# Optimization experiments

Measured on AMD Instinct MI355X. Metric: run time of the kernel, lower is better.

## Reference

```python
import jax, jax.numpy as jnp
import numpy as np

N = 50000   # vertices
E = 25000   # hyperedges
NNZ = 400000  # incidence pairs (v, e)
D_IN = 512
D_OUT = 512  # heads * out_channels, heads=1


def setup_inputs() -> dict:
    key = jax.random.key(0)
    kx, kw, kv, ke = jax.random.split(key, 4)
    X = jax.random.normal(kx, (N, D_IN), dtype=jnp.float32)
    W = jax.random.normal(kw, (D_OUT, D_IN), dtype=jnp.float32) * 0.02  # nn.Linear weight [out,in]
    vidx = jax.random.randint(kv, (NNZ,), 0, N, dtype=jnp.int32)
    eidx = jax.random.randint(ke, (NNZ,), 0, E, dtype=jnp.int32)
    # degE = 1/|e| (hyperedge size), degV = 1/deg(v), as precomputed by hyperg
    ones = jnp.ones((NNZ,), dtype=jnp.float32)
    edge_sz = jax.ops.segment_sum(ones, eidx, num_segments=E)
    vert_dg = jax.ops.segment_sum(ones, vidx, num_segments=N)
    degE = 1.0 / jnp.maximum(edge_sz, 1.0)
    degV = 1.0 / jnp.maximum(vert_dg, 1.0)
    Wdiag = jnp.ones((E,), dtype=jnp.float32)
    return {"X": X, "W": W, "degE": degE, "degV": degV, "Wdiag": Wdiag,
            "vidx": vidx, "eidx": eidx}


def reference(X, W, degE, degV, Wdiag, vidx, eidx):
    # Dense projection: X @ W^T (nn.Linear, no bias)
    Xp = jnp.einsum('nd,od->no', X, W)                      # [N, D_OUT]
    # Stage 1: vertex -> hyperedge (first_aggr: mean via degE), weighted by Wdiag
    Xe = jax.ops.segment_sum(Xp[vidx], eidx, num_segments=E)  # [E, D_OUT]
    Xe = Xe * (degE * Wdiag)[:, None]
    # Stage 2: hyperedge -> vertex, normalized by degV
    Xv = jax.ops.segment_sum(Xe[eidx], vidx, num_segments=N)  # [N, D_OUT]
    Xv = Xv * degV[:, None]
    return Xv
```

## Files before the change

kernel.cpp:

```cpp
#include <hip/hip_runtime.h>

typedef unsigned short u16;
typedef unsigned int   u32;
typedef __attribute__((ext_vector_type(4))) float f32x4;
typedef __attribute__((ext_vector_type(4))) u32   u32x4;
typedef __attribute__((ext_vector_type(8))) __bf16 bf16x8;

constexpr int NV   = 50000;
constexpr int NE   = 25000;
constexpr int NNZp = 400000;
constexpr int D    = 512;
constexpr int MP2  = 25088;
constexpr int NBE  = 25;
constexpr int NBV  = 49;
constexpr int SG1  = 391;
constexpr int SG2  = 1563;

static __device__ __forceinline__ u16 f2bf(float f) {
  u32 u = __float_as_uint(f);
  u32 r = (u + 0x7fffu + ((u >> 16) & 1u)) >> 16;
  return (u16)r;
}
static __device__ __forceinline__ u32 pk2(float a, float b) {
  return (u32)f2bf(a) | ((u32)f2bf(b) << 16);
}

static __device__ __forceinline__ void gload_lds16(const u16* g, u16* l) {
  __builtin_amdgcn_global_load_lds(
      (const __attribute__((address_space(1))) u32*)g,
      (__attribute__((address_space(3))) u32*)l, 16, 0, 0);
}

__global__ void zero_kernel(int* cntE, int* cntV) {
  int i = blockIdx.x * 256 + threadIdx.x;
  if (i < NE) cntE[i] = 0;
  if (i < NV) cntV[i] = 0;
}

__global__ void hist_kernel(const int* __restrict__ vidx, const int* __restrict__ eidx,
                            int* cntE, int* cntV) {
  int i = blockIdx.x * 256 + threadIdx.x;
  if (i < NNZp) {
    atomicAdd(&cntE[eidx[i]], 1);
    atomicAdd(&cntV[vidx[i]], 1);
  }
}

__global__ __launch_bounds__(256) void scan1_kernel(
    const int* __restrict__ cntE, const int* __restrict__ cntV,
    int* offE, int* offV, int* blkSum) {
  const bool isE = blockIdx.x < NBE;
  const int* cnt = isE ? cntE : cntV;
  int* off = isE ? offE : offV;
  const int len = isE ? NE : NV;
  const int t = threadIdx.x;
  const int base = (isE ? blockIdx.x : blockIdx.x - NBE) * 1024 + t * 4;
  int4 c = {0, 0, 0, 0};
  if (base + 4 <= len) c = *(const int4*)(cnt + base);
  else {
    if (base + 0 < len) c.x = cnt[base + 0];
    if (base + 1 < len) c.y = cnt[base + 1];
    if (base + 2 < len) c.z = cnt[base + 2];
    if (base + 3 < len) c.w = cnt[base + 3];
  }
  int s = c.x + c.y + c.z + c.w;
  __shared__ int sm[256];
  sm[t] = s;
  __syncthreads();
  for (int d = 1; d < 256; d <<= 1) {
    int u = (t >= d) ? sm[t - d] : 0;
    __syncthreads();
    sm[t] += u;
    __syncthreads();
  }
  int ex = sm[t] - s;
  int4 o;
  o.x = ex; o.y = o.x + c.x; o.z = o.y + c.y; o.w = o.z + c.z;
  if (base + 4 <= len) *(int4*)(off + base) = o;
  else {
    if (base + 0 < len) off[base + 0] = o.x;
    if (base + 1 < len) off[base + 1] = o.y;
    if (base + 2 < len) off[base + 2] = o.z;
    if (base + 3 < len) off[base + 3] = o.w;
  }
  if (t == 255) blkSum[blockIdx.x] = sm[255];
}

__global__ void scan2_kernel(int* blkSum) {
  int wv = threadIdx.x >> 6, lane = threadIdx.x & 63;
  int off = wv ? NBE : 0, len = wv ? NBV : NBE;
  int v = (lane < len) ? blkSum[off + lane] : 0;
  int incl = v;
#pragma unroll
  for (int d = 1; d < 64; d <<= 1) {
    int u = __shfl_up(incl, d, 64);
    if (lane >= d) incl += u;
  }
  if (lane < len) blkSum[off + lane] = incl - v;
}

__global__ __launch_bounds__(256) void scan3_kernel(
    int* offE, int* offV, int* curE, int* curV, const int* __restrict__ blkSum) {
  const bool isE = blockIdx.x < NBE;
  int* off = isE ? offE : offV;
  int* cur = isE ? curE : curV;
  const int len = isE ? NE : NV;
  const int pref = blkSum[blockIdx.x];
  const int base = (isE ? blockIdx.x : blockIdx.x - NBE) * 1024 + threadIdx.x * 4;
  if (base + 4 <= len) {
    int4 o = *(int4*)(off + base);
    o.x += pref; o.y += pref; o.z += pref; o.w += pref;
    *(int4*)(off + base) = o;
    *(int4*)(cur + base) = o;
  } else {
    for (int q = 0; q < 4; q++)
      if (base + q < len) { int v = off[base + q] + pref; off[base + q] = v; cur[base + q] = v; }
  }
}

__global__ void scatter_kernel(const int* __restrict__ vidx, const int* __restrict__ eidx,
                               int* curE, int* curV, int* csr_ev, int* csr_ve) {
  int i = blockIdx.x * 256 + threadIdx.x;
  if (i < NNZp) {
    int e = eidx[i], v = vidx[i];
    csr_ev[atomicAdd(&curE[e], 1)] = v;
    csr_ve[atomicAdd(&curV[v], 1)] = e;
  }
}

__global__ __launch_bounds__(256) void convert_kernel(
    const float* __restrict__ X, const float* __restrict__ W,
    u16* __restrict__ Xb, u16* __restrict__ Wb) {
  constexpr size_t NX = (size_t)NV * D;
  size_t i = ((size_t)blockIdx.x * 256 + threadIdx.x) * 8;
  const float* src;
  u16* dst;
  if (i < NX) {
    int n = (int)(i >> 9);
    int col = (int)(i & 511);
    int t = col >> 5, w = col & 31;
    src = X + i;
    dst = Xb + (size_t)t * NV * 32 + (size_t)n * 32 + w;
  } else {
    src = W + (i - NX);
    dst = Wb + (i - NX);
  }
  f32x4 a = *(const f32x4*)src;
  f32x4 b = *(const f32x4*)(src + 4);
  u32x4 p = { pk2(a[0], a[1]), pk2(a[2], a[3]), pk2(b[0], b[1]), pk2(b[2], b[3]) };
  *(u32x4*)dst = p;
}

__global__ __launch_bounds__(256) void stage1_kernel(
    const u16* __restrict__ Xb, const int* __restrict__ offE, const int* __restrict__ cntE,
    const int* __restrict__ csr_ev, u16* __restrict__ XeR) {
  const int wave = threadIdx.x >> 6;
  const int lane = threadIdx.x & 63;
  const int g    = lane >> 2;
  const int c    = lane & 3;
  const int bid  = blockIdx.x;
  const int xcd  = bid & 7;
  const int tmp  = bid >> 3;
  const int phase = (tmp >= SG1) ? 1 : 0;
  const int sg    = tmp - phase * SG1;
  const int t     = xcd + 8 * phase;
  const int e     = sg * 64 + wave * 16 + g;
  const u16* base = Xb + (size_t)t * NV * 32;
  int start = 0, cnt = 0;
  if (e < NE) { start = offE[e]; cnt = cntE[e]; }
  float acc[8] = {};
  for (int j0 = 0; j0 < cnt; j0 += 4) {
    int idx = (j0 + c < cnt) ? csr_ev[start + j0 + c] : 0;
    int kmax = min(4, cnt - j0);
    for (int k = 0; k < kmax; k++) {
      int v = __shfl(idx, (lane & ~3) | k, 64);
      u32x4 p = *(const u32x4*)(base + (size_t)v * 32 + c * 8);
#pragma unroll
      for (int q = 0; q < 4; q++) {
        u32 u = p[q];
        acc[2 * q]     += __uint_as_float(u << 16);
        acc[2 * q + 1] += __uint_as_float(u & 0xffff0000u);
      }
    }
  }
  if (e < NE) {
    u32x4 o = { pk2(acc[0], acc[1]), pk2(acc[2], acc[3]),
                pk2(acc[4], acc[5]), pk2(acc[6], acc[7]) };
    *(u32x4*)(XeR + (size_t)e * D + t * 32 + c * 8) = o;
  }
}

__global__ __launch_bounds__(256) void gemm_kernel(const u16* __restrict__ A,
                                                   const u16* __restrict__ B,
                                                   const float* __restrict__ degE,
                                                   const float* __restrict__ Wdiag,
                                                   u16* __restrict__ C) {
  __shared__ u16 sA[128 * 32];
  __shared__ u16 sB[128 * 32];
  const int tid  = threadIdx.x;
  const int lane = tid & 63;
  const int wave = tid >> 6;
  const int bm = blockIdx.y * 128;
  const int bn = blockIdx.x * 128;
  const int wm = (wave >> 1) * 64;
  const int wn = (wave & 1) * 64;
  const int lr = lane & 15;
  const int lk = (lane >> 4) * 8;
  const int srow = lane >> 2;
  const int scol = (lane & 3) * 8;

  f32x4 acc[4][4] = {};

  for (int kt = 0; kt < D; kt += 32) {
    __syncthreads();
#pragma unroll
    for (int c = 0; c < 2; c++) {
      const int ar = wave * 16 + c * 64;
      gload_lds16(A + (size_t)(bm + ar + srow) * D + kt + scol, &sA[ar * 32]);
      gload_lds16(B + (size_t)(bn + ar + srow) * D + kt + scol, &sB[ar * 32]);
    }
    __syncthreads();

    bf16x8 af[4], bfr[4];
#pragma unroll
    for (int i = 0; i < 4; i++) af[i]  = *(const bf16x8*)&sA[(wm + i * 16 + lr) * 32 + lk];
#pragma unroll
    for (int j = 0; j < 4; j++) bfr[j] = *(const bf16x8*)&sB[(wn + j * 16 + lr) * 32 + lk];
#pragma unroll
    for (int i = 0; i < 4; i++)
#pragma unroll
      for (int j = 0; j < 4; j++)
        acc[i][j] = __builtin_amdgcn_mfma_f32_16x16x32_bf16(af[i], bfr[j], acc[i][j], 0, 0, 0);
  }

#pragma unroll
  for (int i = 0; i < 4; i++)
#pragma unroll
    for (int r = 0; r < 4; r++) {
      int row = bm + wm + i * 16 + (lane >> 4) * 4 + r;
      if (row < NE) {
        float se = degE[row] * Wdiag[row];
#pragma unroll
        for (int j = 0; j < 4; j++) {
          int col = bn + wn + lr + j * 16;
          int s = col >> 6, w = col & 63;
          C[(size_t)s * MP2 * 64 + (size_t)row * 64 + w] = f2bf(acc[i][j][r] * se);
        }
      }
    }
}

__global__ __launch_bounds__(256) void stage2_kernel(
    const u16* __restrict__ Xe2, const int* __restrict__ offV, const int* __restrict__ cntV,
    const int* __restrict__ csr_ve, const float* __restrict__ degV, float* __restrict__ out) {
  const int wave = threadIdx.x >> 6;
  const int lane = threadIdx.x & 63;
  const int g    = lane >> 3;
  const int c    = lane & 7;
  const int s    = blockIdx.x & 7;
  const int sg   = blockIdx.x >> 3;
  const int v    = sg * 32 + wave * 8 + g;
  const u16* base = Xe2 + (size_t)s * MP2 * 64;
  int start = 0, cnt = 0;
  if (v < NV) { start = offV[v]; cnt = cntV[v]; }
  float acc[8] = {};
  for (int j0 = 0; j0 < cnt; j0 += 8) {
    int idx = (j0 + c < cnt) ? csr_ve[start + j0 + c] : 0;
    int kmax = min(8, cnt - j0);
    for (int k = 0; k < kmax; k++) {
      int e = __shfl(idx, (lane & ~7) | k, 64);
      u32x4 p = *(const u32x4*)(base + (size_t)e * 64 + c * 8);
#pragma unroll
      for (int q = 0; q < 4; q++) {
        u32 u = p[q];
        acc[2 * q]     += __uint_as_float(u << 16);
        acc[2 * q + 1] += __uint_as_float(u & 0xffff0000u);
      }
    }
  }
  if (v < NV) {
    float sc = degV[v];
    float* orow = out + (size_t)v * D + s * 64 + c * 8;
    f32x4 o0 = { acc[0] * sc, acc[1] * sc, acc[2] * sc, acc[3] * sc };
    f32x4 o1 = { acc[4] * sc, acc[5] * sc, acc[6] * sc, acc[7] * sc };
    *(f32x4*)orow = o0;
    *(f32x4*)(orow + 4) = o1;
  }
}

extern "C" void kernel_launch(void* const* d_in, const int* in_sizes, int n_in,
                              void* d_out, int out_size, void* d_ws, size_t ws_size,
                              hipStream_t stream) {
  const float* X     = (const float*)d_in[0];
  const float* W     = (const float*)d_in[1];
  const float* degE  = (const float*)d_in[2];
  const float* degV  = (const float*)d_in[3];
  const float* Wdiag = (const float*)d_in[4];
  const int*   vidx  = (const int*)d_in[5];
  const int*   eidx  = (const int*)d_in[6];
  float* out = (float*)d_out;

  char* p = (char*)d_ws;
  auto take = [&](size_t bytes) { char* r = p; p += (bytes + 255) & ~(size_t)255; return r; };
  u16* Xb     = (u16*)take((size_t)NV * D * 2);
  u16* Wb     = (u16*)take((size_t)D * D * 2);
  u16* XeR    = (u16*)take((size_t)MP2 * D * 2);
  u16* Xe2    = (u16*)take((size_t)MP2 * D * 2);
  int* cntE   = (int*)take((size_t)NE * 4);
  int* offE   = (int*)take((size_t)NE * 4);
  int* curE   = (int*)take((size_t)NE * 4);
  int* cntV   = (int*)take((size_t)NV * 4);
  int* offV   = (int*)take((size_t)NV * 4);
  int* curV   = (int*)take((size_t)NV * 4);
  int* csr_ev = (int*)take((size_t)NNZp * 4);
  int* csr_ve = (int*)take((size_t)NNZp * 4);
  int* blkSum = (int*)take((size_t)(NBE + NBV) * 4);

  constexpr size_t NCONV = ((size_t)NV * D + (size_t)D * D) / 8 / 256;

  zero_kernel   <<<(NV + 255) / 256, 256, 0, stream>>>(cntE, cntV);
  hist_kernel   <<<(NNZp + 255) / 256, 256, 0, stream>>>(vidx, eidx, cntE, cntV);
  scan1_kernel  <<<NBE + NBV, 256, 0, stream>>>(cntE, cntV, offE, offV, blkSum);
  scan2_kernel  <<<1, 128, 0, stream>>>(blkSum);
  scan3_kernel  <<<NBE + NBV, 256, 0, stream>>>(offE, offV, curE, curV, blkSum);
  scatter_kernel<<<(NNZp + 255) / 256, 256, 0, stream>>>(vidx, eidx, curE, curV, csr_ev, csr_ve);
  convert_kernel<<<NCONV, 256, 0, stream>>>(X, W, Xb, Wb);
  stage1_kernel <<<SG1 * 16, 256, 0, stream>>>(Xb, offE, cntE, csr_ev, XeR);
  gemm_kernel   <<<dim3(D / 128, MP2 / 128), 256, 0, stream>>>(XeR, Wb, degE, Wdiag, Xe2);
  stage2_kernel <<<SG2 * 8, 256, 0, stream>>>(Xe2, offV, cntV, csr_ve, degV, out);
}
```

Baseline: 434.2 us.

## Use row-major layouts and one-wave-per-row gathers with batched loads

Drops the column-slab tiled layouts of Xb and Xe2 in favour of plain row-major storage. Each wave now handles one hyperedge or vertex, and its 64 lanes cover the full 512-wide row, so every gathered row is one contiguous 1 KB read. Eight gathered rows are loaded into registers before accumulating, to keep more memory requests in flight. The cost is that the slab layout, which kept each XCD's working set to one column slice for L2 locality, is gone, and per-row load imbalance now falls on whole waves.

```diff
diff --git a/kernel.cpp b/kernel.cpp
--- a/kernel.cpp
+++ b/kernel.cpp
@@ -13,8 +13,6 @@
 constexpr int MP2  = 25088;
 constexpr int NBE  = 25;
 constexpr int NBV  = 49;
-constexpr int SG1  = 391;
-constexpr int SG2  = 1563;
 
 static __device__ __forceinline__ u16 f2bf(float f) {
   u32 u = __float_as_uint(f);
@@ -136,11 +134,8 @@
   const float* src;
   u16* dst;
   if (i < NX) {
-    int n = (int)(i >> 9);
-    int col = (int)(i & 511);
-    int t = col >> 5, w = col & 31;
     src = X + i;
-    dst = Xb + (size_t)t * NV * 32 + (size_t)n * 32 + w;
+    dst = Xb + i;
   } else {
     src = W + (i - NX);
     dst = Wb + (i - NX);
@@ -156,38 +151,59 @@
     const int* __restrict__ csr_ev, u16* __restrict__ XeR) {
   const int wave = threadIdx.x >> 6;
   const int lane = threadIdx.x & 63;
-  const int g    = lane >> 2;
-  const int c    = lane & 3;
-  const int bid  = blockIdx.x;
-  const int xcd  = bid & 7;
-  const int tmp  = bid >> 3;
-  const int phase = (tmp >= SG1) ? 1 : 0;
-  const int sg    = tmp - phase * SG1;
-  const int t     = xcd + 8 * phase;
-  const int e     = sg * 64 + wave * 16 + g;
-  const u16* base = Xb + (size_t)t * NV * 32;
-  int start = 0, cnt = 0;
-  if (e < NE) { start = offE[e]; cnt = cntE[e]; }
+  const int e = blockIdx.x * 4 + wave;
+  if (e >= NE) return;
+  const int start = offE[e];
+  const int cnt   = cntE[e];
   float acc[8] = {};
-  for (int j0 = 0; j0 < cnt; j0 += 4) {
-    int idx = (j0 + c < cnt) ? csr_ev[start + j0 + c] : 0;
-    int kmax = min(4, cnt - j0);
-    for (int k = 0; k < kmax; k++) {
-      int v = __shfl(idx, (lane & ~3) | k, 64);
-      u32x4 p = *(const u32x4*)(base + (size_t)v * 32 + c * 8);
-#pragma unroll
-      for (int q = 0; q < 4; q++) {
-        u32 u = p[q];
-        acc[2 * q]     += __uint_as_float(u << 16);
-        acc[2 * q + 1] += __uint_as_float(u & 0xffff0000u);
-      }
-    }
-  }
-  if (e < NE) {
-    u32x4 o = { pk2(acc[0], acc[1]), pk2(acc[2], acc[3]),
-                pk2(acc[4], acc[5]), pk2(acc[6], acc[7]) };
-    *(u32x4*)(XeR + (size_t)e * D + t * 32 + c * 8) = o;
-  }
+  for (int b = 0; b < cnt; b += 64) {
+    const int n = min(64, cnt - b);
+    int idx = 0;
+    if (lane < n) idx = csr_ev[start + b + lane];
+    int k0 = 0;
+    for (; k0 + 8 <= n; k0 += 8) {
+      u32x4 buf[8];
+#pragma unroll
+      for (int p = 0; p < 8; p++) {
+        int v = __shfl(idx, k0 + p, 64);
+        buf[p] = *(const u32x4*)(Xb + (size_t)v * D + lane * 8);
+      }
+#pragma unroll
+      for (int p = 0; p < 8; p++) {
+#pragma unroll
+        for (int q = 0; q < 4; q++) {
+          u32 u = buf[p][q];
+          acc[2 * q]     += __uint_as_float(u << 16);
+          acc[2 * q + 1] += __uint_as_float(u & 0xffff0000u);
+        }
+      }
+    }
+    const int rem = n - k0;
+    if (rem) {
+      u32x4 buf[8];
+#pragma unroll
+      for (int p = 0; p < 8; p++) {
+        if (p < rem) {
+          int v = __shfl(idx, k0 + p, 64);
+          buf[p] = *(const u32x4*)(Xb + (size_t)v * D + lane * 8);
+        }
+      }
+#pragma unroll
+      for (int p = 0; p < 8; p++) {
+        if (p < rem) {
+#pragma unroll
+          for (int q = 0; q < 4; q++) {
+            u32 u = buf[p][q];
+            acc[2 * q]     += __uint_as_float(u << 16);
+            acc[2 * q + 1] += __uint_as_float(u & 0xffff0000u);
+          }
+        }
+      }
+    }
+  }
+  u32x4 o = { pk2(acc[0], acc[1]), pk2(acc[2], acc[3]),
+              pk2(acc[4], acc[5]), pk2(acc[6], acc[7]) };
+  *(u32x4*)(XeR + (size_t)e * D + lane * 8) = o;
 }
 
 __global__ __launch_bounds__(256) void gemm_kernel(const u16* __restrict__ A,
@@ -243,8 +259,7 @@
 #pragma unroll
         for (int j = 0; j < 4; j++) {
           int col = bn + wn + lr + j * 16;
-          int s = col >> 6, w = col & 63;
-          C[(size_t)s * MP2 * 64 + (size_t)row * 64 + w] = f2bf(acc[i][j][r] * se);
+          C[(size_t)row * D + col] = f2bf(acc[i][j][r] * se);
         }
       }
     }
@@ -255,37 +270,62 @@
     const int* __restrict__ csr_ve, const float* __restrict__ degV, float* __restrict__ out) {
   const int wave = threadIdx.x >> 6;
   const int lane = threadIdx.x & 63;
-  const int g    = lane >> 3;
-  const int c    = lane & 7;
-  const int s    = blockIdx.x & 7;
-  const int sg   = blockIdx.x >> 3;
-  const int v    = sg * 32 + wave * 8 + g;
-  const u16* base = Xe2 + (size_t)s * MP2 * 64;
-  int start = 0, cnt = 0;
-  if (v < NV) { start = offV[v]; cnt = cntV[v]; }
+  const int v = blockIdx.x * 4 + wave;
+  if (v >= NV) return;
+  const int start = offV[v];
+  const int cnt   = cntV[v];
   float acc[8] = {};
-  for (int j0 = 0; j0 < cnt; j0 += 8) {
-    int idx = (j0 + c < cnt) ? csr_ve[start + j0 + c] : 0;
-    int kmax = min(8, cnt - j0);
-    for (int k = 0; k < kmax; k++) {
-      int e = __shfl(idx, (lane & ~7) | k, 64);
-      u32x4 p = *(const u32x4*)(base + (size_t)e * 64 + c * 8);
-#pragma unroll
-      for (int q = 0; q < 4; q++) {
-        u32 u = p[q];
-        acc[2 * q]     += __uint_as_float(u << 16);
-        acc[2 * q + 1] += __uint_as_float(u & 0xffff0000u);
-      }
-    }
-  }
-  if (v < NV) {
-    float sc = degV[v];
-    float* orow = out + (size_t)v * D + s * 64 + c * 8;
-    f32x4 o0 = { acc[0] * sc, acc[1] * sc, acc[2] * sc, acc[3] * sc };
-    f32x4 o1 = { acc[4] * sc, acc[5] * sc, acc[6] * sc, acc[7] * sc };
-    *(f32x4*)orow = o0;
-    *(f32x4*)(orow + 4) = o1;
-  }
+  for (int b = 0; b < cnt; b += 64) {
+    const int n = min(64, cnt - b);
+    int idx = 0;
+    if (lane < n) idx = csr_ve[start + b + lane];
+    int k0 = 0;
+    for (; k0 + 8 <= n; k0 += 8) {
+      u32x4 buf[8];
+#pragma unroll
+      for (int p = 0; p < 8; p++) {
+        int e = __shfl(idx, k0 + p, 64);
+        buf[p] = *(const u32x4*)(Xe2 + (size_t)e * D + lane * 8);
+      }
+#pragma unroll
+      for (int p = 0; p < 8; p++) {
+#pragma unroll
+        for (int q = 0; q < 4; q++) {
+          u32 u = buf[p][q];
+          acc[2 * q]     += __uint_as_float(u << 16);
+          acc[2 * q + 1] += __uint_as_float(u & 0xffff0000u);
+        }
+      }
+    }
+    const int rem = n - k0;
+    if (rem) {
+      u32x4 buf[8];
+#pragma unroll
+      for (int p = 0; p < 8; p++) {
+        if (p < rem) {
+          int e = __shfl(idx, k0 + p, 64);
+          buf[p] = *(const u32x4*)(Xe2 + (size_t)e * D + lane * 8);
+        }
+      }
+#pragma unroll
+      for (int p = 0; p < 8; p++) {
+        if (p < rem) {
+#pragma unroll
+          for (int q = 0; q < 4; q++) {
+            u32 u = buf[p][q];
+            acc[2 * q]     += __uint_as_float(u << 16);
+            acc[2 * q + 1] += __uint_as_float(u & 0xffff0000u);
+          }
+        }
+      }
+    }
+  }
+  const float sc = degV[v];
+  float* orow = out + (size_t)v * D + lane * 8;
+  f32x4 o0 = { acc[0] * sc, acc[1] * sc, acc[2] * sc, acc[3] * sc };
+  f32x4 o1 = { acc[4] * sc, acc[5] * sc, acc[6] * sc, acc[7] * sc };
+  *(f32x4*)orow = o0;
+  *(f32x4*)(orow + 4) = o1;
 }
 
 extern "C" void kernel_launch(void* const* d_in, const int* in_sizes, int n_in,
@@ -325,7 +365,7 @@
   scan3_kernel  <<<NBE + NBV, 256, 0, stream>>>(offE, offV, curE, curV, blkSum);
   scatter_kernel<<<(NNZp + 255) / 256, 256, 0, stream>>>(vidx, eidx, curE, curV, csr_ev, csr_ve);
   convert_kernel<<<NCONV, 256, 0, stream>>>(X, W, Xb, Wb);
-  stage1_kernel <<<SG1 * 16, 256, 0, stream>>>(Xb, offE, cntE, csr_ev, XeR);
+  stage1_kernel <<<NE / 4, 256, 0, stream>>>(Xb, offE, cntE, csr_ev, XeR);
   gemm_kernel   <<<dim3(D / 128, MP2 / 128), 256, 0, stream>>>(XeR, Wb, degE, Wdiag, Xe2);
-  stage2_kernel <<<SG2 * 8, 256, 0, stream>>>(Xe2, offV, cntV, csr_ve, degV, out);
-}
+  stage2_kernel <<<NV / 4, 256, 0, stream>>>(Xe2, offV, cntV, csr_ve, degV, out);
+}
```

Measured after the change: 429.8 us. Within noise of the previous version (-1.0%).

## Assign one wave per segment in gather stages with cross-lane butterfly reduction

Applied to the files above, without the earlier changes.

Stage1 and stage2 now give each wave a single hyperedge or vertex instead of 16 or 8 segments per wave. The wave's lane groups walk different neighbours in parallel, and the partial sums are combined with a shfl_xor butterfly reduction that also transposes the columns so each lane stores one scalar. This is meant to remove serial per-segment loops and load imbalance from varying segment sizes, and to raise memory-level parallelism. In exchange it adds shuffle work, turns the vector stores into scalar stores, launches many more blocks, drops the bounds checks on e and v, and uses nontemporal loads for the CSR index arrays.

```diff
diff --git a/kernel.cpp b/kernel.cpp
--- a/kernel.cpp
+++ b/kernel.cpp
@@ -13,8 +13,7 @@
 constexpr int MP2  = 25088;
 constexpr int NBE  = 25;
 constexpr int NBV  = 49;
-constexpr int SG1  = 391;
-constexpr int SG2  = 1563;
+constexpr int EB1  = 6250;
 
 static __device__ __forceinline__ u16 f2bf(float f) {
   u32 u = __float_as_uint(f);
@@ -156,24 +155,23 @@
     const int* __restrict__ csr_ev, u16* __restrict__ XeR) {
   const int wave = threadIdx.x >> 6;
   const int lane = threadIdx.x & 63;
-  const int g    = lane >> 2;
+  const int slot = lane >> 2;
   const int c    = lane & 3;
   const int bid  = blockIdx.x;
   const int xcd  = bid & 7;
   const int tmp  = bid >> 3;
-  const int phase = (tmp >= SG1) ? 1 : 0;
-  const int sg    = tmp - phase * SG1;
+  const int phase = (tmp >= EB1) ? 1 : 0;
+  const int eg    = tmp - phase * EB1;
   const int t     = xcd + 8 * phase;
-  const int e     = sg * 64 + wave * 16 + g;
+  const int e     = eg * 4 + wave;
+  const int start = __builtin_nontemporal_load(offE + e);
+  const int cnt   = __builtin_nontemporal_load(cntE + e);
   const u16* base = Xb + (size_t)t * NV * 32;
-  int start = 0, cnt = 0;
-  if (e < NE) { start = offE[e]; cnt = cntE[e]; }
   float acc[8] = {};
-  for (int j0 = 0; j0 < cnt; j0 += 4) {
-    int idx = (j0 + c < cnt) ? csr_ev[start + j0 + c] : 0;
-    int kmax = min(4, cnt - j0);
-    for (int k = 0; k < kmax; k++) {
-      int v = __shfl(idx, (lane & ~3) | k, 64);
+  for (int j0 = 0; j0 < cnt; j0 += 16) {
+    int j = j0 + slot;
+    if (j < cnt) {
+      int v = __builtin_nontemporal_load(csr_ev + start + j);
       u32x4 p = *(const u32x4*)(base + (size_t)v * 32 + c * 8);
 #pragma unroll
       for (int q = 0; q < 4; q++) {
@@ -183,10 +181,27 @@
       }
     }
   }
-  if (e < NE) {
-    u32x4 o = { pk2(acc[0], acc[1]), pk2(acc[2], acc[3]),
-                pk2(acc[4], acc[5]), pk2(acc[6], acc[7]) };
-    *(u32x4*)(XeR + (size_t)e * D + t * 32 + c * 8) = o;
+#pragma unroll
+  for (int i = 0; i < 4; i++) {
+    float send = (lane & 4) ? acc[i] : acc[i + 4];
+    float keep = (lane & 4) ? acc[i + 4] : acc[i];
+    acc[i] = keep + __shfl_xor(send, 4, 64);
+  }
+#pragma unroll
+  for (int i = 0; i < 2; i++) {
+    float send = (lane & 8) ? acc[i] : acc[i + 2];
+    float keep = (lane & 8) ? acc[i + 2] : acc[i];
+    acc[i] = keep + __shfl_xor(send, 8, 64);
+  }
+  {
+    float send = (lane & 16) ? acc[0] : acc[1];
+    float keep = (lane & 16) ? acc[1] : acc[0];
+    acc[0] = keep + __shfl_xor(send, 16, 64);
+  }
+  acc[0] += __shfl_xor(acc[0], 32, 64);
+  if (!(lane & 32)) {
+    int col = c * 8 + ((lane >> 2) & 1) * 4 + ((lane >> 3) & 1) * 2 + ((lane >> 4) & 1);
+    XeR[(size_t)e * D + t * 32 + col] = f2bf(acc[0]);
   }
 }
 
@@ -255,20 +270,19 @@
     const int* __restrict__ csr_ve, const float* __restrict__ degV, float* __restrict__ out) {
   const int wave = threadIdx.x >> 6;
   const int lane = threadIdx.x & 63;
-  const int g    = lane >> 3;
+  const int slot = lane >> 3;
   const int c    = lane & 7;
   const int s    = blockIdx.x & 7;
-  const int sg   = blockIdx.x >> 3;
-  const int v    = sg * 32 + wave * 8 + g;
+  const int vg   = blockIdx.x >> 3;
+  const int v    = vg * 4 + wave;
+  const int start = __builtin_nontemporal_load(offV + v);
+  const int cnt   = __builtin_nontemporal_load(cntV + v);
   const u16* base = Xe2 + (size_t)s * MP2 * 64;
-  int start = 0, cnt = 0;
-  if (v < NV) { start = offV[v]; cnt = cntV[v]; }
   float acc[8] = {};
   for (int j0 = 0; j0 < cnt; j0 += 8) {
-    int idx = (j0 + c < cnt) ? csr_ve[start + j0 + c] : 0;
-    int kmax = min(8, cnt - j0);
-    for (int k = 0; k < kmax; k++) {
-      int e = __shfl(idx, (lane & ~7) | k, 64);
+    int j = j0 + slot;
+    if (j < cnt) {
+      int e = __builtin_nontemporal_load(csr_ve + start + j);
       u32x4 p = *(const u32x4*)(base + (size_t)e * 64 + c * 8);
 #pragma unroll
       for (int q = 0; q < 4; q++) {
@@ -278,14 +292,26 @@
       }
     }
   }
-  if (v < NV) {
-    float sc = degV[v];
-    float* orow = out + (size_t)v * D + s * 64 + c * 8;
-    f32x4 o0 = { acc[0] * sc, acc[1] * sc, acc[2] * sc, acc[3] * sc };
-    f32x4 o1 = { acc[4] * sc, acc[5] * sc, acc[6] * sc, acc[7] * sc };
-    *(f32x4*)orow = o0;
-    *(f32x4*)(orow + 4) = o1;
-  }
+#pragma unroll
+  for (int i = 0; i < 4; i++) {
+    float send = (lane & 8) ? acc[i] : acc[i + 4];
+    float keep = (lane & 8) ? acc[i + 4] : acc[i];
+    acc[i] = keep + __shfl_xor(send, 8, 64);
+  }
+#pragma unroll
+  for (int i = 0; i < 2; i++) {
+    float send = (lane & 16) ? acc[i] : acc[i + 2];
+    float keep = (lane & 16) ? acc[i + 2] : acc[i];
+    acc[i] = keep + __shfl_xor(send, 16, 64);
+  }
+  {
+    float send = (lane & 32) ? acc[0] : acc[1];
+    float keep = (lane & 32) ? acc[1] : acc[0];
+    acc[0] = keep + __shfl_xor(send, 32, 64);
+  }
+  const float sc = degV[v];
+  int col = c * 8 + ((lane >> 3) & 1) * 4 + ((lane >> 4) & 1) * 2 + ((lane >> 5) & 1);
+  out[(size_t)v * D + s * 64 + col] = acc[0] * sc;
 }
 
 extern "C" void kernel_launch(void* const* d_in, const int* in_sizes, int n_in,
@@ -325,7 +351,7 @@
   scan3_kernel  <<<NBE + NBV, 256, 0, stream>>>(offE, offV, curE, curV, blkSum);
   scatter_kernel<<<(NNZp + 255) / 256, 256, 0, stream>>>(vidx, eidx, curE, curV, csr_ev, csr_ve);
   convert_kernel<<<NCONV, 256, 0, stream>>>(X, W, Xb, Wb);
-  stage1_kernel <<<SG1 * 16, 256, 0, stream>>>(Xb, offE, cntE, csr_ev, XeR);
+  stage1_kernel <<<EB1 * 16, 256, 0, stream>>>(Xb, offE, cntE, csr_ev, XeR);
   gemm_kernel   <<<dim3(D / 128, MP2 / 128), 256, 0, stream>>>(XeR, Wb, degE, Wdiag, Xe2);
-  stage2_kernel <<<SG2 * 8, 256, 0, stream>>>(Xe2, offV, cntV, csr_ve, degV, out);
-}
+  stage2_kernel <<<(NV / 4) * 8, 256, 0, stream>>>(Xe2, offV, cntV, csr_ve, degV, out);
+}
```

Result: slower. 619.6 us (+42.7%).

## Sort rows by degree for load-balanced gathers and batch neighbor index loads

Applied to the files above, without the earlier changes.

Adds a degree histogram, a scan and a counting-sort pass so hyperedges and vertices are processed in degree-sorted order. Rows with similar neighbor counts then share a wave, which is meant to reduce divergence in the stage1 and stage2 gather loops. The inner loops also change: each lane now loads 4 indices directly and issues 4 independent row loads at a time instead of shuffling one index per step, which exposes more memory-level parallelism. The cost is extra small kernels and indirect id lookups, and output writes become scattered rather than in row order.

```diff
diff --git a/kernel.cpp b/kernel.cpp
--- a/kernel.cpp
+++ b/kernel.cpp
@@ -13,8 +13,8 @@
 constexpr int MP2  = 25088;
 constexpr int NBE  = 25;
 constexpr int NBV  = 49;
-constexpr int SG1  = 391;
-constexpr int SG2  = 1563;
+constexpr int BPS1 = 391;
+constexpr int BPS2 = 1563;
 
 static __device__ __forceinline__ u16 f2bf(float f) {
   u32 u = __float_as_uint(f);
@@ -31,10 +31,11 @@
       (__attribute__((address_space(3))) u32*)l, 16, 0, 0);
 }
 
-__global__ void zero_kernel(int* cntE, int* cntV) {
+__global__ void zero_kernel(int* cntE, int* cntV, int* dhistE, int* dhistV) {
   int i = blockIdx.x * 256 + threadIdx.x;
   if (i < NE) cntE[i] = 0;
   if (i < NV) cntV[i] = 0;
+  if (i < 64) { dhistE[i] = 0; dhistV[i] = 0; }
 }
 
 __global__ void hist_kernel(const int* __restrict__ vidx, const int* __restrict__ eidx,
@@ -44,6 +45,20 @@
     atomicAdd(&cntE[eidx[i]], 1);
     atomicAdd(&cntV[vidx[i]], 1);
   }
+}
+
+__global__ __launch_bounds__(256) void deghist_kernel(
+    const int* __restrict__ cntE, const int* __restrict__ cntV, int* dhistE, int* dhistV) {
+  __shared__ int lhE[64], lhV[64];
+  int t = threadIdx.x;
+  if (t < 64) { lhE[t] = 0; lhV[t] = 0; }
+  __syncthreads();
+  int i = blockIdx.x * 256 + t;
+  if (i < NE) atomicAdd(&lhE[min(cntE[i], 63)], 1);
+  if (i < NV) atomicAdd(&lhV[min(cntV[i], 63)], 1);
+  __syncthreads();
+  if (t < 64) { if (lhE[t]) atomicAdd(&dhistE[t], lhE[t]); }
+  else if (t < 128) { int u = t - 64; if (lhV[u]) atomicAdd(&dhistV[u], lhV[u]); }
 }
 
 __global__ __launch_bounds__(256) void scan1_kernel(
@@ -86,17 +101,22 @@
   if (t == 255) blkSum[blockIdx.x] = sm[255];
 }
 
-__global__ void scan2_kernel(int* blkSum) {
+__global__ void scan2_kernel(int* blkSum, const int* __restrict__ dhistE,
+                             const int* __restrict__ dhistV, int* dcurE, int* dcurV) {
   int wv = threadIdx.x >> 6, lane = threadIdx.x & 63;
-  int off = wv ? NBE : 0, len = wv ? NBV : NBE;
-  int v = (lane < len) ? blkSum[off + lane] : 0;
+  const int* s; int* d; int len;
+  if (wv == 0)      { s = blkSum;       d = blkSum;       len = NBE; }
+  else if (wv == 1) { s = blkSum + NBE; d = blkSum + NBE; len = NBV; }
+  else if (wv == 2) { s = dhistE;       d = dcurE;        len = 64;  }
+  else              { s = dhistV;       d = dcurV;        len = 64;  }
+  int v = (lane < len) ? s[lane] : 0;
   int incl = v;
 #pragma unroll
-  for (int d = 1; d < 64; d <<= 1) {
-    int u = __shfl_up(incl, d, 64);
-    if (lane >= d) incl += u;
-  }
-  if (lane < len) blkSum[off + lane] = incl - v;
+  for (int dd = 1; dd < 64; dd <<= 1) {
+    int u = __shfl_up(incl, dd, 64);
+    if (lane >= dd) incl += u;
+  }
+  if (lane < len) d[lane] = incl - v;
 }
 
 __global__ __launch_bounds__(256) void scan3_kernel(
@@ -128,6 +148,34 @@
   }
 }
 
+__global__ __launch_bounds__(256) void degsort_kernel(
+    const int* __restrict__ cntE, const int* __restrict__ offE,
+    const int* __restrict__ cntV, const int* __restrict__ offV,
+    const float* __restrict__ degV, int* dcurE, int* dcurV,
+    int* sE_id, int* sE_off, int* sE_cnt,
+    int* sV_id, int* sV_off, int* sV_cnt, float* sV_deg) {
+  __shared__ int lhE[64], lhV[64], lbE[64], lbV[64];
+  int t = threadIdx.x;
+  if (t < 64) { lhE[t] = 0; lhV[t] = 0; }
+  __syncthreads();
+  int i = blockIdx.x * 256 + t;
+  int bE = 0, rE = 0, bV = 0, rV = 0;
+  if (i < NE) { bE = min(cntE[i], 63); rE = atomicAdd(&lhE[bE], 1); }
+  if (i < NV) { bV = min(cntV[i], 63); rV = atomicAdd(&lhV[bV], 1); }
+  __syncthreads();
+  if (t < 64) { lbE[t] = lhE[t] ? atomicAdd(&dcurE[t], lhE[t]) : 0; }
+  else if (t < 128) { int u = t - 64; lbV[u] = lhV[u] ? atomicAdd(&dcurV[u], lhV[u]) : 0; }
+  __syncthreads();
+  if (i < NE) {
+    int r = lbE[bE] + rE;
+    sE_id[r] = i; sE_off[r] = offE[i]; sE_cnt[r] = cntE[i];
+  }
+  if (i < NV) {
+    int r = lbV[bV] + rV;
+    sV_id[r] = i; sV_off[r] = offV[i]; sV_cnt[r] = cntV[i]; sV_deg[r] = degV[i];
+  }
+}
+
 __global__ __launch_bounds__(256) void convert_kernel(
     const float* __restrict__ X, const float* __restrict__ W,
     u16* __restrict__ Xb, u16* __restrict__ Wb) {
@@ -152,8 +200,8 @@
 }
 
 __global__ __launch_bounds__(256) void stage1_kernel(
-    const u16* __restrict__ Xb, const int* __restrict__ offE, const int* __restrict__ cntE,
-    const int* __restrict__ csr_ev, u16* __restrict__ XeR) {
+    const u16* __restrict__ Xb, const int* __restrict__ sE_off, const int* __restrict__ sE_cnt,
+    const int* __restrict__ sE_id, const int* __restrict__ csr_ev, u16* __restrict__ XeR) {
   const int wave = threadIdx.x >> 6;
   const int lane = threadIdx.x & 63;
   const int g    = lane >> 2;
@@ -161,29 +209,46 @@
   const int bid  = blockIdx.x;
   const int xcd  = bid & 7;
   const int tmp  = bid >> 3;
-  const int phase = (tmp >= SG1) ? 1 : 0;
-  const int sg    = tmp - phase * SG1;
+  const int phase = (tmp >= BPS1) ? 1 : 0;
+  const int eg    = tmp - phase * BPS1;
   const int t     = xcd + 8 * phase;
-  const int e     = sg * 64 + wave * 16 + g;
+  const int rank  = eg * 64 + wave * 16 + g;
   const u16* base = Xb + (size_t)t * NV * 32;
-  int start = 0, cnt = 0;
-  if (e < NE) { start = offE[e]; cnt = cntE[e]; }
+  int start = 0, cnt = 0, e = 0;
+  if (rank < NE) {
+    start = __builtin_nontemporal_load(sE_off + rank);
+    cnt   = __builtin_nontemporal_load(sE_cnt + rank);
+    e     = __builtin_nontemporal_load(sE_id + rank);
+  }
   float acc[8] = {};
-  for (int j0 = 0; j0 < cnt; j0 += 4) {
-    int idx = (j0 + c < cnt) ? csr_ev[start + j0 + c] : 0;
-    int kmax = min(4, cnt - j0);
-    for (int k = 0; k < kmax; k++) {
-      int v = __shfl(idx, (lane & ~3) | k, 64);
-      u32x4 p = *(const u32x4*)(base + (size_t)v * 32 + c * 8);
+  int j0 = 0;
+  for (; j0 + 4 <= cnt; j0 += 4) {
+    int idx[4];
+#pragma unroll
+    for (int p = 0; p < 4; p++) idx[p] = __builtin_nontemporal_load(csr_ev + start + j0 + p);
+    u32x4 pk[4];
+#pragma unroll
+    for (int p = 0; p < 4; p++) pk[p] = *(const u32x4*)(base + (size_t)idx[p] * 32 + c * 8);
+#pragma unroll
+    for (int p = 0; p < 4; p++)
 #pragma unroll
       for (int q = 0; q < 4; q++) {
-        u32 u = p[q];
+        u32 u = pk[p][q];
         acc[2 * q]     += __uint_as_float(u << 16);
         acc[2 * q + 1] += __uint_as_float(u & 0xffff0000u);
       }
+  }
+  for (; j0 < cnt; j0++) {
+    int v = __builtin_nontemporal_load(csr_ev + start + j0);
+    u32x4 p = *(const u32x4*)(base + (size_t)v * 32 + c * 8);
+#pragma unroll
+    for (int q = 0; q < 4; q++) {
+      u32 u = p[q];
+      acc[2 * q]     += __uint_as_float(u << 16);
+      acc[2 * q + 1] += __uint_as_float(u & 0xffff0000u);
     }
   }
-  if (e < NE) {
+  if (rank < NE) {
     u32x4 o = { pk2(acc[0], acc[1]), pk2(acc[2], acc[3]),
                 pk2(acc[4], acc[5]), pk2(acc[6], acc[7]) };
     *(u32x4*)(XeR + (size_t)e * D + t * 32 + c * 8) = o;
@@ -251,38 +316,57 @@
 }
 
 __global__ __launch_bounds__(256) void stage2_kernel(
-    const u16* __restrict__ Xe2, const int* __restrict__ offV, const int* __restrict__ cntV,
-    const int* __restrict__ csr_ve, const float* __restrict__ degV, float* __restrict__ out) {
+    const u16* __restrict__ Xe2, const int* __restrict__ sV_off, const int* __restrict__ sV_cnt,
+    const int* __restrict__ sV_id, const float* __restrict__ sV_deg,
+    const int* __restrict__ csr_ve, float* __restrict__ out) {
   const int wave = threadIdx.x >> 6;
   const int lane = threadIdx.x & 63;
   const int g    = lane >> 3;
   const int c    = lane & 7;
   const int s    = blockIdx.x & 7;
-  const int sg   = blockIdx.x >> 3;
-  const int v    = sg * 32 + wave * 8 + g;
+  const int vg   = blockIdx.x >> 3;
+  const int rank = vg * 32 + wave * 8 + g;
   const u16* base = Xe2 + (size_t)s * MP2 * 64;
-  int start = 0, cnt = 0;
-  if (v < NV) { start = offV[v]; cnt = cntV[v]; }
+  int start = 0, cnt = 0, v = 0;
+  float dv = 0.f;
+  if (rank < NV) {
+    start = __builtin_nontemporal_load(sV_off + rank);
+    cnt   = __builtin_nontemporal_load(sV_cnt + rank);
+    v     = __builtin_nontemporal_load(sV_id + rank);
+    dv    = __builtin_nontemporal_load(sV_deg + rank);
+  }
   float acc[8] = {};
-  for (int j0 = 0; j0 < cnt; j0 += 8) {
-    int idx = (j0 + c < cnt) ? csr_ve[start + j0 + c] : 0;
-    int kmax = min(8, cnt - j0);
-    for (int k = 0; k < kmax; k++) {
-      int e = __shfl(idx, (lane & ~7) | k, 64);
-      u32x4 p = *(const u32x4*)(base + (size_t)e * 64 + c * 8);
+  int j0 = 0;
+  for (; j0 + 4 <= cnt; j0 += 4) {
+    int idx[4];
+#pragma unroll
+    for (int p = 0; p < 4; p++) idx[p] = __builtin_nontemporal_load(csr_ve + start + j0 + p);
+    u32x4 pk[4];
+#pragma unroll
+    for (int p = 0; p < 4; p++) pk[p] = *(const u32x4*)(base + (size_t)idx[p] * 64 + c * 8);
+#pragma unroll
+    for (int p = 0; p < 4; p++)
 #pragma unroll
       for (int q = 0; q < 4; q++) {
-        u32 u = p[q];
+        u32 u = pk[p][q];
         acc[2 * q]     += __uint_as_float(u << 16);
         acc[2 * q + 1] += __uint_as_float(u & 0xffff0000u);
       }
+  }
+  for (; j0 < cnt; j0++) {
+    int e = __builtin_nontemporal_load(csr_ve + start + j0);
+    u32x4 p = *(const u32x4*)(base + (size_t)e * 64 + c * 8);
+#pragma unroll
+    for (int q = 0; q < 4; q++) {
+      u32 u = p[q];
+      acc[2 * q]     += __uint_as_float(u << 16);
+      acc[2 * q + 1] += __uint_as_float(u & 0xffff0000u);
     }
   }
-  if (v < NV) {
-    float sc = degV[v];
+  if (rank < NV) {
     float* orow = out + (size_t)v * D + s * 64 + c * 8;
-    f32x4 o0 = { acc[0] * sc, acc[1] * sc, acc[2] * sc, acc[3] * sc };
-    f32x4 o1 = { acc[4] * sc, acc[5] * sc, acc[6] * sc, acc[7] * sc };
+    f32x4 o0 = { acc[0] * dv, acc[1] * dv, acc[2] * dv, acc[3] * dv };
+    f32x4 o1 = { acc[4] * dv, acc[5] * dv, acc[6] * dv, acc[7] * dv };
     *(f32x4*)orow = o0;
     *(f32x4*)(orow + 4) = o1;
   }
@@ -315,17 +399,32 @@
   int* csr_ev = (int*)take((size_t)NNZp * 4);
   int* csr_ve = (int*)take((size_t)NNZp * 4);
   int* blkSum = (int*)take((size_t)(NBE + NBV) * 4);
+  int* dhistE = (int*)take(64 * 4);
+  int* dhistV = (int*)take(64 * 4);
+  int* dcurE  = (int*)take(64 * 4);
+  int* dcurV  = (int*)take(64 * 4);
+  int* sE_id  = (int*)take((size_t)NE * 4);
+  int* sE_off = (int*)take((size_t)NE * 4);
+  int* sE_cnt = (int*)take((size_t)NE * 4);
+  int* sV_id  = (int*)take((size_t)NV * 4);
+  int* sV_off = (int*)take((size_t)NV * 4);
+  int* sV_cnt = (int*)take((size_t)NV * 4);
+  float* sV_deg = (float*)take((size_t)NV * 4);
 
   constexpr size_t NCONV = ((size_t)NV * D + (size_t)D * D) / 8 / 256;
-
-  zero_kernel   <<<(NV + 255) / 256, 256, 0, stream>>>(cntE, cntV);
+  constexpr int NSEG = (NV + 255) / 256;
+
+  zero_kernel   <<<NSEG, 256, 0, stream>>>(cntE, cntV, dhistE, dhistV);
   hist_kernel   <<<(NNZp + 255) / 256, 256, 0, stream>>>(vidx, eidx, cntE, cntV);
+  deghist_kernel<<<NSEG, 256, 0, stream>>>(cntE, cntV, dhistE, dhistV);
   scan1_kernel  <<<NBE + NBV, 256, 0, stream>>>(cntE, cntV, offE, offV, blkSum);
-  scan2_kernel  <<<1, 128, 0, stream>>>(blkSum);
+  scan2_kernel  <<<1, 256, 0, stream>>>(blkSum, dhistE, dhistV, dcurE, dcurV);
   scan3_kernel  <<<NBE + NBV, 256, 0, stream>>>(offE, offV, curE, curV, blkSum);
   scatter_kernel<<<(NNZp + 255) / 256, 256, 0, stream>>>(vidx, eidx, curE, curV, csr_ev, csr_ve);
+  degsort_kernel<<<NSEG, 256, 0, stream>>>(cntE, offE, cntV, offV, degV, dcurE, dcurV,
+                                           sE_id, sE_off, sE_cnt, sV_id, sV_off, sV_cnt, sV_deg);
   convert_kernel<<<NCONV, 256, 0, stream>>>(X, W, Xb, Wb);
-  stage1_kernel <<<SG1 * 16, 256, 0, stream>>>(Xb, offE, cntE, csr_ev, XeR);
+  stage1_kernel <<<BPS1 * 16, 256, 0, stream>>>(Xb, sE_off, sE_cnt, sE_id, csr_ev, XeR);
   gemm_kernel   <<<dim3(D / 128, MP2 / 128), 256, 0, stream>>>(XeR, Wb, degE, Wdiag, Xe2);
-  stage2_kernel <<<SG2 * 8, 256, 0, stream>>>(Xe2, offV, cntV, csr_ve, degV, out);
-}
+  stage2_kernel <<<BPS2 * 8, 256, 0, stream>>>(Xe2, sV_off, sV_cnt, sV_id, sV_deg, csr_ve, out);
+}
```

Result: slower. 516.9 us (+19.0%).
